# Optimization experiments

Hardware: AMD Instinct MI355X
Metric: run time of the kernel (lower is better)

Reference implementation:

```python
import jax, jax.numpy as jnp
import numpy as np


def setup_inputs() -> dict:
    key = jax.random.key(0)
    k1, k2, k3 = jax.random.split(key, 3)
    T, H, E = 16384, 4096, 64  # tokens, hidden_size, num_experts
    x = jax.random.normal(k1, (T, H), dtype=jnp.float32)
    weight = jax.random.normal(k2, (E, H), dtype=jnp.float32) * (1.0 / np.sqrt(H))
    bias = jax.random.normal(k3, (E,), dtype=jnp.float32) * 0.01
    return {"x": x, "weight": weight, "bias": bias}


def reference(x, weight, bias):
    TOP_K = 8
    # logits: [T, E] = x @ weight.T + bias
    logits = jnp.einsum("th,eh->te", x, weight) + bias
    top_values, top_indices = jax.lax.top_k(logits, TOP_K)  # [T, K]
    top_weights = jax.nn.softmax(top_values, axis=-1)
    return (top_weights, top_indices)
```

## Files before the change

kernel.cpp:

```cpp
#include <hip/hip_runtime.h>
#include <float.h>
#include <math.h>

#define TOKS 16384
#define HDIM 4096
#define NEXP 64
#define BM   64
#define BK   64
#define NCH  (HDIM / BK)

typedef __attribute__((ext_vector_type(8)))  short short8v;
typedef __attribute__((ext_vector_type(16))) float f32x16;

__device__ __forceinline__ void split3(float v, unsigned& b1, unsigned& b2, unsigned& b3) {
  unsigned xb = __float_as_uint(v);
  b1 = xb >> 16;
  float r = v - __uint_as_float(xb & 0xFFFF0000u);
  unsigned rb = __float_as_uint(r);
  b2 = rb >> 16;
  float r2 = r - __uint_as_float(rb & 0xFFFF0000u);
  b3 = __float_as_uint(r2) >> 16;
}

__device__ __forceinline__ void cvt2(float a, float b, unsigned& o1, unsigned& o2, unsigned& o3) {
  unsigned a1, a2, a3, c1, c2, c3;
  split3(a, a1, a2, a3);
  split3(b, c1, c2, c3);
  o1 = a1 | (c1 << 16); o2 = a2 | (c2 << 16); o3 = a3 | (c3 << 16);
}

__global__ __launch_bounds__(256)
void router_mfma_kernel(const float* __restrict__ x,
                        const float* __restrict__ wgt,
                        const float* __restrict__ bias,
                        float* __restrict__ out) {
  __shared__ __align__(16) unsigned char smem[114688];
  const int tid  = threadIdx.x;
  const int lane = tid & 63;
  const int wv   = tid >> 6;
  const int tokBase = blockIdx.x * BM;

  const int stok = tid >> 2;
  const int seg  = tid & 3;
  const unsigned swz0 = (unsigned)(((seg * 2)     ^ (stok & 7)) << 4);
  const unsigned swz1 = (unsigned)(((seg * 2 + 1) ^ (stok & 7)) << 4);
  const int rowbyte_s = stok * 128;
  const float* const xrow = x   + (size_t)(tokBase + stok) * HDIM;
  const float* const wrow = wgt + (size_t)stok * HDIM;

  const int wm = wv >> 1, we = wv & 1;
  const int r  = lane & 31, h2 = lane >> 5;
  const int r7 = r & 7;
  const int byteA = (wm * 32 + r) * 128;
  const int byteB = (we * 32 + r) * 128;

  f32x16 acc_m0, acc_m1, acc_c;
#pragma unroll
  for (int i = 0; i < 16; ++i) { acc_m0[i] = 0.f; acc_m1[i] = 0.f; acc_c[i] = 0.f; }

  float4 nf0, nf1, nf2, nf3;
  float4 ng0, ng1, ng2, ng3;

#define GLOAD(c) do { \
    const int kb_ = (c) * BK + seg * 16; \
    nf0 = *(const float4*)(xrow + kb_);      nf1 = *(const float4*)(xrow + kb_ + 4); \
    nf2 = *(const float4*)(xrow + kb_ + 8);  nf3 = *(const float4*)(xrow + kb_ + 12); \
    ng0 = *(const float4*)(wrow + kb_);      ng1 = *(const float4*)(wrow + kb_ + 4); \
    ng2 = *(const float4*)(wrow + kb_ + 8);  ng3 = *(const float4*)(wrow + kb_ + 12); \
  } while (0)

#define SWRITE(b) do { \
    unsigned char* bb_ = smem + (b) * 49152; \
    uint4 q1l, q2l, q3l, q1h, q2h, q3h; \
    cvt2(nf0.x, nf0.y, q1l.x, q2l.x, q3l.x); \
    cvt2(nf0.z, nf0.w, q1l.y, q2l.y, q3l.y); \
    cvt2(nf1.x, nf1.y, q1l.z, q2l.z, q3l.z); \
    cvt2(nf1.z, nf1.w, q1l.w, q2l.w, q3l.w); \
    cvt2(nf2.x, nf2.y, q1h.x, q2h.x, q3h.x); \
    cvt2(nf2.z, nf2.w, q1h.y, q2h.y, q3h.y); \
    cvt2(nf3.x, nf3.y, q1h.z, q2h.z, q3h.z); \
    cvt2(nf3.z, nf3.w, q1h.w, q2h.w, q3h.w); \
    *(uint4*)(bb_ +     0 + rowbyte_s + swz0) = q1l; \
    *(uint4*)(bb_ +     0 + rowbyte_s + swz1) = q1h; \
    *(uint4*)(bb_ +  8192 + rowbyte_s + swz0) = q2l; \
    *(uint4*)(bb_ +  8192 + rowbyte_s + swz1) = q2h; \
    *(uint4*)(bb_ + 16384 + rowbyte_s + swz0) = q3l; \
    *(uint4*)(bb_ + 16384 + rowbyte_s + swz1) = q3h; \
    cvt2(ng0.x, ng0.y, q1l.x, q2l.x, q3l.x); \
    cvt2(ng0.z, ng0.w, q1l.y, q2l.y, q3l.y); \
    cvt2(ng1.x, ng1.y, q1l.z, q2l.z, q3l.z); \
    cvt2(ng1.z, ng1.w, q1l.w, q2l.w, q3l.w); \
    cvt2(ng2.x, ng2.y, q1h.x, q2h.x, q3h.x); \
    cvt2(ng2.z, ng2.w, q1h.y, q2h.y, q3h.y); \
    cvt2(ng3.x, ng3.y, q1h.z, q2h.z, q3h.z); \
    cvt2(ng3.z, ng3.w, q1h.w, q2h.w, q3h.w); \
    *(uint4*)(bb_ + 24576 + rowbyte_s + swz0) = q1l; \
    *(uint4*)(bb_ + 24576 + rowbyte_s + swz1) = q1h; \
    *(uint4*)(bb_ + 32768 + rowbyte_s + swz0) = q2l; \
    *(uint4*)(bb_ + 32768 + rowbyte_s + swz1) = q2h; \
    *(uint4*)(bb_ + 40960 + rowbyte_s + swz0) = q3l; \
    *(uint4*)(bb_ + 40960 + rowbyte_s + swz1) = q3h; \
  } while (0)

#define MFMA(a, b, c) __builtin_amdgcn_mfma_f32_32x32x16_bf16((a), (b), (c), 0, 0, 0)

#define COMPUTE(b) do { \
    const unsigned char* bb_ = smem + (b) * 49152; \
    _Pragma("unroll") \
    for (int s = 0; s < 4; ++s) { \
      const int off_ = ((2 * s + h2) ^ r7) << 4; \
      const short8v a1_ = *(const short8v*)(bb_ +     0 + byteA + off_); \
      const short8v b1_ = *(const short8v*)(bb_ + 24576 + byteB + off_); \
      if (s < 2) acc_m0 = MFMA(a1_, b1_, acc_m0); \
      else       acc_m1 = MFMA(a1_, b1_, acc_m1); \
      const short8v a2_ = *(const short8v*)(bb_ +  8192 + byteA + off_); \
      const short8v b2_ = *(const short8v*)(bb_ + 32768 + byteB + off_); \
      acc_c = MFMA(a1_, b2_, acc_c); \
      acc_c = MFMA(a2_, b1_, acc_c); \
      const short8v a3_ = *(const short8v*)(bb_ + 16384 + byteA + off_); \
      const short8v b3_ = *(const short8v*)(bb_ + 40960 + byteB + off_); \
      acc_c = MFMA(a1_, b3_, acc_c); \
      acc_c = MFMA(a2_, b2_, acc_c); \
      acc_c = MFMA(a3_, b1_, acc_c); \
    } \
  } while (0)

  GLOAD(0);
  SWRITE(0);
  __syncthreads();
  for (int c = 0; c < NCH; ++c) {
    if (c < NCH - 1) GLOAD(c + 1);
    COMPUTE(c & 1);
    __syncthreads();
    if (c < NCH - 1) SWRITE((c + 1) & 1);
    __syncthreads();
  }

  float* fin = (float*)(smem + 98304);
#pragma unroll
  for (int reg = 0; reg < 16; ++reg) {
    const int rowf = (reg & 3) + 8 * (reg >> 2) + 4 * h2;
    fin[(wm * 32 + rowf) * 64 + we * 32 + r] = (acc_m0[reg] + acc_m1[reg]) + acc_c[reg];
  }
  __syncthreads();

  for (int tt = 0; tt < 16; ++tt) {
    const int t = wv * 16 + tt;
    float v = fin[t * 64 + lane] + bias[lane];
    float myval = 0.f, m0 = 0.f;
    int myidx = 0;
#pragma unroll
    for (int k = 0; k < 8; ++k) {
      float bv = v;
      int   bi = lane;
#pragma unroll
      for (int off = 1; off < 64; off <<= 1) {
        const float ov = __shfl_xor(bv, off);
        const int   oi = __shfl_xor(bi, off);
        if (ov > bv || (ov == bv && oi < bi)) { bv = ov; bi = oi; }
      }
      if (k == 0) m0 = bv;
      if (lane == k) { myval = bv; myidx = bi; }
      if (lane == bi) v = -FLT_MAX;
    }
    const float el = (lane < 8) ? expf(myval - m0) : 0.f;
    float ssum = el;
    ssum += __shfl_xor(ssum, 1);
    ssum += __shfl_xor(ssum, 2);
    ssum += __shfl_xor(ssum, 4);
    if (lane < 8) {
      const size_t tg = (size_t)(tokBase + t);
      out[tg * 8 + lane] = el / ssum;
      out[(size_t)TOKS * 8 + tg * 8 + lane] = (float)myidx;
    }
  }
}

extern "C" void kernel_launch(void* const* d_in, const int* in_sizes, int n_in,
                              void* d_out, int out_size, void* d_ws, size_t ws_size,
                              hipStream_t stream) {
  const float* x    = (const float*)d_in[0];
  const float* wgt  = (const float*)d_in[1];
  const float* bias = (const float*)d_in[2];
  float* out = (float*)d_out;
  hipLaunchKernelGGL(router_mfma_kernel, dim3(TOKS / BM), dim3(256), 0, stream,
                     x, wgt, bias, out);
}
```

Before: 171.0 us.

## Split K across blocks with partial sums and a separate reduce+top-k kernel

Adds a grid dimension that splits the hidden dimension into up to 3 K-slices, chosen from the workspace size. Each block writes its partial logits tile to workspace, and a new kernel sums the partials and runs the top-k/softmax. The shared-memory buffer shrinks from a double buffer to a single buffer, so more blocks can be resident per CU. This targets the low occupancy of one 64-token block per CU. The cost is extra partial-sum traffic, a second launch, and losing the overlap that double buffering gave.

```diff
diff --git a/kernel.cpp b/kernel.cpp
--- a/kernel.cpp
+++ b/kernel.cpp
@@ -29,16 +29,55 @@
   o1 = a1 | (c1 << 16); o2 = a2 | (c2 << 16); o3 = a3 | (c3 << 16);
 }
 
+__device__ __forceinline__ void topk_softmax(const float* fin, const float* __restrict__ bias,
+                                             float* __restrict__ out, int tokBase,
+                                             int lane, int wv) {
+  for (int tt = 0; tt < 16; ++tt) {
+    const int t = wv * 16 + tt;
+    float v = fin[t * 64 + lane] + bias[lane];
+    float myval = 0.f, m0 = 0.f;
+    int myidx = 0;
+#pragma unroll
+    for (int k = 0; k < 8; ++k) {
+      float bv = v;
+      int   bi = lane;
+#pragma unroll
+      for (int off = 1; off < 64; off <<= 1) {
+        const float ov = __shfl_xor(bv, off);
+        const int   oi = __shfl_xor(bi, off);
+        if (ov > bv || (ov == bv && oi < bi)) { bv = ov; bi = oi; }
+      }
+      if (k == 0) m0 = bv;
+      if (lane == k) { myval = bv; myidx = bi; }
+      if (lane == bi) v = -FLT_MAX;
+    }
+    const float el = (lane < 8) ? expf(myval - m0) : 0.f;
+    float ssum = el;
+    ssum += __shfl_xor(ssum, 1);
+    ssum += __shfl_xor(ssum, 2);
+    ssum += __shfl_xor(ssum, 4);
+    if (lane < 8) {
+      const size_t tg = (size_t)(tokBase + t);
+      out[tg * 8 + lane] = el / ssum;
+      out[(size_t)TOKS * 8 + tg * 8 + lane] = (float)myidx;
+    }
+  }
+}
+
 __global__ __launch_bounds__(256)
 void router_mfma_kernel(const float* __restrict__ x,
                         const float* __restrict__ wgt,
                         const float* __restrict__ bias,
-                        float* __restrict__ out) {
-  __shared__ __align__(16) unsigned char smem[114688];
+                        float* __restrict__ out,
+                        float* __restrict__ part, int ks) {
+  __shared__ __align__(16) unsigned char smem[49152];
   const int tid  = threadIdx.x;
   const int lane = tid & 63;
   const int wv   = tid >> 6;
+  const int kt   = blockIdx.y;
   const int tokBase = blockIdx.x * BM;
+  const int cStart = (NCH * kt) / ks;
+  const int cEnd   = (NCH * (kt + 1)) / ks;
 
   const int stok = tid >> 2;
   const int seg  = tid & 3;
@@ -69,8 +108,8 @@
     ng2 = *(const float4*)(wrow + kb_ + 8);  ng3 = *(const float4*)(wrow + kb_ + 12); \
   } while (0)
 
-#define SWRITE(b) do { \
-    unsigned char* bb_ = smem + (b) * 49152; \
+#define SWRITE() do { \
+    unsigned char* bb_ = smem; \
     uint4 q1l, q2l, q3l, q1h, q2h, q3h; \
     cvt2(nf0.x, nf0.y, q1l.x, q2l.x, q3l.x); \
     cvt2(nf0.z, nf0.w, q1l.y, q2l.y, q3l.y); \
@@ -104,8 +143,8 @@
 
 #define MFMA(a, b, c) __builtin_amdgcn_mfma_f32_32x32x16_bf16((a), (b), (c), 0, 0, 0)
 
-#define COMPUTE(b) do { \
-    const unsigned char* bb_ = smem + (b) * 49152; \
+#define COMPUTE() do { \
+    const unsigned char* bb_ = smem; \
     _Pragma("unroll") \
     for (int s = 0; s < 4; ++s) { \
       const int off_ = ((2 * s + h2) ^ r7) << 4; \
@@ -125,55 +164,68 @@
     } \
   } while (0)
 
-  GLOAD(0);
-  SWRITE(0);
+  GLOAD(cStart);
+  SWRITE();
   __syncthreads();
-  for (int c = 0; c < NCH; ++c) {
-    if (c < NCH - 1) GLOAD(c + 1);
-    COMPUTE(c & 1);
+  for (int c = cStart; c < cEnd; ++c) {
+    const bool more = (c + 1 < cEnd);
+    if (more) GLOAD(c + 1);
+    COMPUTE();
     __syncthreads();
-    if (c < NCH - 1) SWRITE((c + 1) & 1);
+    if (more) { SWRITE(); __syncthreads(); }
+  }
+
+  if (ks == 1) {
+    float* fin = (float*)smem;
+#pragma unroll
+    for (int reg = 0; reg < 16; ++reg) {
+      const int rowf = (reg & 3) + 8 * (reg >> 2) + 4 * h2;
+      fin[(wm * 32 + rowf) * 64 + we * 32 + r] = (acc_m0[reg] + acc_m1[reg]) + acc_c[reg];
+    }
     __syncthreads();
-  }
-
-  float* fin = (float*)(smem + 98304);
-#pragma unroll
-  for (int reg = 0; reg < 16; ++reg) {
-    const int rowf = (reg & 3) + 8 * (reg >> 2) + 4 * h2;
-    fin[(wm * 32 + rowf) * 64 + we * 32 + r] = (acc_m0[reg] + acc_m1[reg]) + acc_c[reg];
-  }
+    topk_softmax(fin, bias, out, tokBase, lane, wv);
+  } else {
+    float* pp = part + ((size_t)kt * (TOKS / BM) + blockIdx.x) * 4096;
+#pragma unroll
+    for (int reg = 0; reg < 16; ++reg) {
+      const int rowf = (reg & 3) + 8 * (reg >> 2) + 4 * h2;
+      pp[(wm * 32 + rowf) * 64 + we * 32 + r] = (acc_m0[reg] + acc_m1[reg]) + acc_c[reg];
+    }
+  }
+}
+
+__global__ __launch_bounds__(256)
+void reduce_topk_kernel(const float* __restrict__ part,
+                        const float* __restrict__ bias,
+                        float* __restrict__ out, int ks) {
+  __shared__ __align__(16) float fin[4096];
+  const int tid  = threadIdx.x;
+  const int lane = tid & 63;
+  const int wv   = tid >> 6;
+  const int tokBase = blockIdx.x * BM;
+
+  const float* p0 = part + (size_t)blockIdx.x * 4096 + tid * 16;
+  float4 s0 = *(const float4*)(p0);
+  float4 s1 = *(const float4*)(p0 + 4);
+  float4 s2 = *(const float4*)(p0 + 8);
+  float4 s3 = *(const float4*)(p0 + 12);
+  for (int kt = 1; kt < ks; ++kt) {
+    const float* p = p0 + (size_t)kt * ((TOKS / BM) * 4096);
+    const float4 q0 = *(const float4*)(p);
+    const float4 q1 = *(const float4*)(p + 4);
+    const float4 q2 = *(const float4*)(p + 8);
+    const float4 q3 = *(const float4*)(p + 12);
+    s0.x += q0.x; s0.y += q0.y; s0.z += q0.z; s0.w += q0.w;
+    s1.x += q1.x; s1.y += q1.y; s1.z += q1.z; s1.w += q1.w;
+    s2.x += q2.x; s2.y += q2.y; s2.z += q2.z; s2.w += q2.w;
+    s3.x += q3.x; s3.y += q3.y; s3.z += q3.z; s3.w += q3.w;
+  }
+  *(float4*)(&fin[tid * 16])      = s0;
+  *(float4*)(&fin[tid * 16 + 4])  = s1;
+  *(float4*)(&fin[tid * 16 + 8])  = s2;
+  *(float4*)(&fin[tid * 16 + 12]) = s3;
   __syncthreads();
-
-  for (int tt = 0; tt < 16; ++tt) {
-    const int t = wv * 16 + tt;
-    float v = fin[t * 64 + lane] + bias[lane];
-    float myval = 0.f, m0 = 0.f;
-    int myidx = 0;
-#pragma unroll
-    for (int k = 0; k < 8; ++k) {
-      float bv = v;
-      int   bi = lane;
-#pragma unroll
-      for (int off = 1; off < 64; off <<= 1) {
-        const float ov = __shfl_xor(bv, off);
-        const int   oi = __shfl_xor(bi, off);
-        if (ov > bv || (ov == bv && oi < bi)) { bv = ov; bi = oi; }
-      }
-      if (k == 0) m0 = bv;
-      if (lane == k) { myval = bv; myidx = bi; }
-      if (lane == bi) v = -FLT_MAX;
-    }
-    const float el = (lane < 8) ? expf(myval - m0) : 0.f;
-    float ssum = el;
-    ssum += __shfl_xor(ssum, 1);
-    ssum += __shfl_xor(ssum, 2);
-    ssum += __shfl_xor(ssum, 4);
-    if (lane < 8) {
-      const size_t tg = (size_t)(tokBase + t);
-      out[tg * 8 + lane] = el / ssum;
-      out[(size_t)TOKS * 8 + tg * 8 + lane] = (float)myidx;
-    }
-  }
+  topk_softmax(fin, bias, out, tokBase, lane, wv);
 }
 
 extern "C" void kernel_launch(void* const* d_in, const int* in_sizes, int n_in,
@@ -182,7 +234,16 @@
   const float* x    = (const float*)d_in[0];
   const float* wgt  = (const float*)d_in[1];
   const float* bias = (const float*)d_in[2];
-  float* out = (float*)d_out;
-  hipLaunchKernelGGL(router_mfma_kernel, dim3(TOKS / BM), dim3(256), 0, stream,
-                     x, wgt, bias, out);
-}
+  float* out  = (float*)d_out;
+  float* part = (float*)d_ws;
+
+  const size_t planeBytes = (size_t)(TOKS / BM) * 4096 * sizeof(float);
+  const int ks = (ws_size >= 3 * planeBytes) ? 3 : (ws_size >= 2 * planeBytes ? 2 : 1);
+
+  hipLaunchKernelGGL(router_mfma_kernel, dim3(TOKS / BM, ks), dim3(256), 0, stream,
+                     x, wgt, bias, out, part, ks);
+  if (ks > 1) {
+    hipLaunchKernelGGL(reduce_topk_kernel, dim3(TOKS / BM), dim3(256), 0, stream,
+                       part, bias, out, ks);
+  }
+}
```

After: 187.3 us. 1.1x slower.

## Split-K router GEMM with pre-split weights, direct register loads, separate reduce+topk

Applied to the files above, without the earlier changes.

Pre-splits the weight matrix into three bf16 planes in a separate kernel. The main kernel now drops shared memory and loads x straight from global into registers, converting it to bf16 triples in registers. The hidden dimension is split across a second grid axis (up to 4 slices, depending on workspace size), so more blocks run and each finishes sooner. A third kernel sums the partial planes and does the top-k and softmax. This adds two extra launches and workspace round-trips for the partials. x loads are no longer staged and shared through LDS, and each wave now reads its own rows directly.

```diff
diff --git a/kernel.cpp b/kernel.cpp
--- a/kernel.cpp
+++ b/kernel.cpp
@@ -6,8 +6,8 @@
 #define HDIM 4096
 #define NEXP 64
 #define BM   64
-#define BK   64
-#define NCH  (HDIM / BK)
+#define NTILE (TOKS / BM)
+#define WPE  262144
 
 typedef __attribute__((ext_vector_type(8)))  short short8v;
 typedef __attribute__((ext_vector_type(16))) float f32x16;
@@ -21,7 +21,6 @@
   float r2 = r - __uint_as_float(rb & 0xFFFF0000u);
   b3 = __float_as_uint(r2) >> 16;
 }
-
 __device__ __forceinline__ void cvt2(float a, float b, unsigned& o1, unsigned& o2, unsigned& o3) {
   unsigned a1, a2, a3, c1, c2, c3;
   split3(a, a1, a2, a3);
@@ -30,123 +29,116 @@
 }
 
 __global__ __launch_bounds__(256)
+void wsplit_kernel(const float* __restrict__ wgt, unsigned short* __restrict__ wsp) {
+  const int gid  = blockIdx.x * 256 + threadIdx.x;
+  const int base = gid * 8;
+  const float4 f0 = *(const float4*)(wgt + base);
+  const float4 f1 = *(const float4*)(wgt + base + 4);
+  uint4 q1, q2, q3;
+  cvt2(f0.x, f0.y, q1.x, q2.x, q3.x);
+  cvt2(f0.z, f0.w, q1.y, q2.y, q3.y);
+  cvt2(f1.x, f1.y, q1.z, q2.z, q3.z);
+  cvt2(f1.z, f1.w, q1.w, q2.w, q3.w);
+  *(uint4*)(wsp + base)            = q1;
+  *(uint4*)(wsp + WPE + base)      = q2;
+  *(uint4*)(wsp + 2 * WPE + base)  = q3;
+}
+
+__global__ __launch_bounds__(256)
 void router_mfma_kernel(const float* __restrict__ x,
-                        const float* __restrict__ wgt,
-                        const float* __restrict__ bias,
-                        float* __restrict__ out) {
-  __shared__ __align__(16) unsigned char smem[114688];
+                        const unsigned short* __restrict__ wsp,
+                        float* __restrict__ part, int ks) {
   const int tid  = threadIdx.x;
   const int lane = tid & 63;
   const int wv   = tid >> 6;
+  const int kt   = blockIdx.y;
   const int tokBase = blockIdx.x * BM;
-
-  const int stok = tid >> 2;
-  const int seg  = tid & 3;
-  const unsigned swz0 = (unsigned)(((seg * 2)     ^ (stok & 7)) << 4);
-  const unsigned swz1 = (unsigned)(((seg * 2 + 1) ^ (stok & 7)) << 4);
-  const int rowbyte_s = stok * 128;
-  const float* const xrow = x   + (size_t)(tokBase + stok) * HDIM;
-  const float* const wrow = wgt + (size_t)stok * HDIM;
 
   const int wm = wv >> 1, we = wv & 1;
   const int r  = lane & 31, h2 = lane >> 5;
-  const int r7 = r & 7;
-  const int byteA = (wm * 32 + r) * 128;
-  const int byteB = (we * 32 + r) * 128;
+
+  const int kSlice = HDIM / ks;
+  const int kStart = kt * kSlice;
+  const int nst    = kSlice / 16;
+
+  const float*          xp = x   + (size_t)(tokBase + wm * 32 + r) * HDIM + kStart + h2 * 8;
+  const unsigned short* bp = wsp + (size_t)(we * 32 + r) * HDIM + kStart + h2 * 8;
 
   f32x16 acc_m0, acc_m1, acc_c;
 #pragma unroll
   for (int i = 0; i < 16; ++i) { acc_m0[i] = 0.f; acc_m1[i] = 0.f; acc_c[i] = 0.f; }
 
-  float4 nf0, nf1, nf2, nf3;
-  float4 ng0, ng1, ng2, ng3;
+#define MFMA(a, b, c) __builtin_amdgcn_mfma_f32_32x32x16_bf16((a), (b), (c), 0, 0, 0)
 
-#define GLOAD(c) do { \
-    const int kb_ = (c) * BK + seg * 16; \
-    nf0 = *(const float4*)(xrow + kb_);      nf1 = *(const float4*)(xrow + kb_ + 4); \
-    nf2 = *(const float4*)(xrow + kb_ + 8);  nf3 = *(const float4*)(xrow + kb_ + 12); \
-    ng0 = *(const float4*)(wrow + kb_);      ng1 = *(const float4*)(wrow + kb_ + 4); \
-    ng2 = *(const float4*)(wrow + kb_ + 8);  ng3 = *(const float4*)(wrow + kb_ + 12); \
+#define STEP(macc, off) do { \
+    const float4 xa_ = *(const float4*)(xp + (off)); \
+    const float4 xb_ = *(const float4*)(xp + (off) + 4); \
+    const short8v b1_ = *(const short8v*)(bp + (off)); \
+    const short8v b2_ = *(const short8v*)(bp + WPE + (off)); \
+    const short8v b3_ = *(const short8v*)(bp + 2 * WPE + (off)); \
+    uint4 q1_, q2_, q3_; \
+    cvt2(xa_.x, xa_.y, q1_.x, q2_.x, q3_.x); \
+    cvt2(xa_.z, xa_.w, q1_.y, q2_.y, q3_.y); \
+    cvt2(xb_.x, xb_.y, q1_.z, q2_.z, q3_.z); \
+    cvt2(xb_.z, xb_.w, q1_.w, q2_.w, q3_.w); \
+    const short8v a1_ = __builtin_bit_cast(short8v, q1_); \
+    const short8v a2_ = __builtin_bit_cast(short8v, q2_); \
+    const short8v a3_ = __builtin_bit_cast(short8v, q3_); \
+    macc  = MFMA(a1_, b1_, macc); \
+    acc_c = MFMA(a1_, b2_, acc_c); \
+    acc_c = MFMA(a2_, b1_, acc_c); \
+    acc_c = MFMA(a1_, b3_, acc_c); \
+    acc_c = MFMA(a2_, b2_, acc_c); \
+    acc_c = MFMA(a3_, b1_, acc_c); \
   } while (0)
 
-#define SWRITE(b) do { \
-    unsigned char* bb_ = smem + (b) * 49152; \
-    uint4 q1l, q2l, q3l, q1h, q2h, q3h; \
-    cvt2(nf0.x, nf0.y, q1l.x, q2l.x, q3l.x); \
-    cvt2(nf0.z, nf0.w, q1l.y, q2l.y, q3l.y); \
-    cvt2(nf1.x, nf1.y, q1l.z, q2l.z, q3l.z); \
-    cvt2(nf1.z, nf1.w, q1l.w, q2l.w, q3l.w); \
-    cvt2(nf2.x, nf2.y, q1h.x, q2h.x, q3h.x); \
-    cvt2(nf2.z, nf2.w, q1h.y, q2h.y, q3h.y); \
-    cvt2(nf3.x, nf3.y, q1h.z, q2h.z, q3h.z); \
-    cvt2(nf3.z, nf3.w, q1h.w, q2h.w, q3h.w); \
-    *(uint4*)(bb_ +     0 + rowbyte_s + swz0) = q1l; \
-    *(uint4*)(bb_ +     0 + rowbyte_s + swz1) = q1h; \
-    *(uint4*)(bb_ +  8192 + rowbyte_s + swz0) = q2l; \
-    *(uint4*)(bb_ +  8192 + rowbyte_s + swz1) = q2h; \
-    *(uint4*)(bb_ + 16384 + rowbyte_s + swz0) = q3l; \
-    *(uint4*)(bb_ + 16384 + rowbyte_s + swz1) = q3h; \
-    cvt2(ng0.x, ng0.y, q1l.x, q2l.x, q3l.x); \
-    cvt2(ng0.z, ng0.w, q1l.y, q2l.y, q3l.y); \
-    cvt2(ng1.x, ng1.y, q1l.z, q2l.z, q3l.z); \
-    cvt2(ng1.z, ng1.w, q1l.w, q2l.w, q3l.w); \
-    cvt2(ng2.x, ng2.y, q1h.x, q2h.x, q3h.x); \
-    cvt2(ng2.z, ng2.w, q1h.y, q2h.y, q3h.y); \
-    cvt2(ng3.x, ng3.y, q1h.z, q2h.z, q3h.z); \
-    cvt2(ng3.z, ng3.w, q1h.w, q2h.w, q3h.w); \
-    *(uint4*)(bb_ + 24576 + rowbyte_s + swz0) = q1l; \
-    *(uint4*)(bb_ + 24576 + rowbyte_s + swz1) = q1h; \
-    *(uint4*)(bb_ + 32768 + rowbyte_s + swz0) = q2l; \
-    *(uint4*)(bb_ + 32768 + rowbyte_s + swz1) = q2h; \
-    *(uint4*)(bb_ + 40960 + rowbyte_s + swz0) = q3l; \
-    *(uint4*)(bb_ + 40960 + rowbyte_s + swz1) = q3h; \
-  } while (0)
-
-#define MFMA(a, b, c) __builtin_amdgcn_mfma_f32_32x32x16_bf16((a), (b), (c), 0, 0, 0)
-
-#define COMPUTE(b) do { \
-    const unsigned char* bb_ = smem + (b) * 49152; \
-    _Pragma("unroll") \
-    for (int s = 0; s < 4; ++s) { \
-      const int off_ = ((2 * s + h2) ^ r7) << 4; \
-      const short8v a1_ = *(const short8v*)(bb_ +     0 + byteA + off_); \
-      const short8v b1_ = *(const short8v*)(bb_ + 24576 + byteB + off_); \
-      if (s < 2) acc_m0 = MFMA(a1_, b1_, acc_m0); \
-      else       acc_m1 = MFMA(a1_, b1_, acc_m1); \
-      const short8v a2_ = *(const short8v*)(bb_ +  8192 + byteA + off_); \
-      const short8v b2_ = *(const short8v*)(bb_ + 32768 + byteB + off_); \
-      acc_c = MFMA(a1_, b2_, acc_c); \
-      acc_c = MFMA(a2_, b1_, acc_c); \
-      const short8v a3_ = *(const short8v*)(bb_ + 16384 + byteA + off_); \
-      const short8v b3_ = *(const short8v*)(bb_ + 40960 + byteB + off_); \
-      acc_c = MFMA(a1_, b3_, acc_c); \
-      acc_c = MFMA(a2_, b2_, acc_c); \
-      acc_c = MFMA(a3_, b1_, acc_c); \
-    } \
-  } while (0)
-
-  GLOAD(0);
-  SWRITE(0);
-  __syncthreads();
-  for (int c = 0; c < NCH; ++c) {
-    if (c < NCH - 1) GLOAD(c + 1);
-    COMPUTE(c & 1);
-    __syncthreads();
-    if (c < NCH - 1) SWRITE((c + 1) & 1);
-    __syncthreads();
+  for (int s = 0; s < nst; s += 2) {
+    STEP(acc_m0, 0);
+    STEP(acc_m1, 16);
+    xp += 32; bp += 32;
   }
 
-  float* fin = (float*)(smem + 98304);
+  float* pp = part + ((size_t)kt * NTILE + blockIdx.x) * 4096;
 #pragma unroll
   for (int reg = 0; reg < 16; ++reg) {
     const int rowf = (reg & 3) + 8 * (reg >> 2) + 4 * h2;
-    fin[(wm * 32 + rowf) * 64 + we * 32 + r] = (acc_m0[reg] + acc_m1[reg]) + acc_c[reg];
+    pp[(wm * 32 + rowf) * 64 + we * 32 + r] = (acc_m0[reg] + acc_m1[reg]) + acc_c[reg];
   }
+}
+
+__global__ __launch_bounds__(64)
+void reduce_topk_kernel(const float* __restrict__ part,
+                        const float* __restrict__ bias,
+                        float* __restrict__ out, int ks) {
+  __shared__ __align__(16) float fin[1024];
+  const int lane = threadIdx.x;
+  const int g    = blockIdx.x;
+  const int tile = g >> 2;
+  const int rowBase = (g & 3) * 16;
+
+  const int row = lane >> 2;
+  const int e0  = (lane & 3) * 16;
+  const size_t off0 = (size_t)tile * 4096 + (rowBase + row) * 64 + e0;
+  float4 s0 = make_float4(0.f, 0.f, 0.f, 0.f), s1 = s0, s2 = s0, s3 = s0;
+  for (int kt = 0; kt < ks; ++kt) {
+    const float* p = part + (size_t)kt * (NTILE * 4096) + off0;
+    const float4 q0 = *(const float4*)(p);
+    const float4 q1 = *(const float4*)(p + 4);
+    const float4 q2 = *(const float4*)(p + 8);
+    const float4 q3 = *(const float4*)(p + 12);
+    s0.x += q0.x; s0.y += q0.y; s0.z += q0.z; s0.w += q0.w;
+    s1.x += q1.x; s1.y += q1.y; s1.z += q1.z; s1.w += q1.w;
+    s2.x += q2.x; s2.y += q2.y; s2.z += q2.z; s2.w += q2.w;
+    s3.x += q3.x; s3.y += q3.y; s3.z += q3.z; s3.w += q3.w;
+  }
+  *(float4*)(&fin[lane * 16])      = s0;
+  *(float4*)(&fin[lane * 16 + 4])  = s1;
+  *(float4*)(&fin[lane * 16 + 8])  = s2;
+  *(float4*)(&fin[lane * 16 + 12]) = s3;
   __syncthreads();
 
   for (int tt = 0; tt < 16; ++tt) {
-    const int t = wv * 16 + tt;
-    float v = fin[t * 64 + lane] + bias[lane];
+    float v = fin[tt * 64 + lane] + bias[lane];
     float myval = 0.f, m0 = 0.f;
     int myidx = 0;
 #pragma unroll
@@ -169,7 +161,7 @@
     ssum += __shfl_xor(ssum, 2);
     ssum += __shfl_xor(ssum, 4);
     if (lane < 8) {
-      const size_t tg = (size_t)(tokBase + t);
+      const size_t tg = (size_t)g * 16 + tt;
       out[tg * 8 + lane] = el / ssum;
       out[(size_t)TOKS * 8 + tg * 8 + lane] = (float)myidx;
     }
@@ -182,7 +174,20 @@
   const float* x    = (const float*)d_in[0];
   const float* wgt  = (const float*)d_in[1];
   const float* bias = (const float*)d_in[2];
-  float* out = (float*)d_out;
-  hipLaunchKernelGGL(router_mfma_kernel, dim3(TOKS / BM), dim3(256), 0, stream,
-                     x, wgt, bias, out);
+  float* out  = (float*)d_out;
+  float* part = (float*)d_ws;
+
+  const size_t planeB = (size_t)NTILE * 4096 * sizeof(float);
+  const size_t wB     = (size_t)3 * WPE * sizeof(unsigned short);
+  int ks = 1;
+  if (ws_size >= 4 * planeB + wB)      ks = 4;
+  else if (ws_size >= 2 * planeB + wB) ks = 2;
+  unsigned short* wsp = (unsigned short*)((char*)d_ws + (size_t)ks * planeB);
+
+  hipLaunchKernelGGL(wsplit_kernel, dim3(NEXP * HDIM / (256 * 8)), dim3(256), 0, stream,
+                     wgt, wsp);
+  hipLaunchKernelGGL(router_mfma_kernel, dim3(NTILE, ks), dim3(256), 0, stream,
+                     x, wsp, part, ks);
+  hipLaunchKernelGGL(reduce_topk_kernel, dim3(TOKS / 16), dim3(64), 0, stream,
+                     part, bias, out, ks);
 }
```

New measurement: 264.7 us. +54.8%, slower.
